# Kernel tuning notes

Measured on AMD Instinct MI355X. Metric: run time of the kernel, lower is better.

The kernel has to match this reference:

```python
import jax, jax.numpy as jnp
import numpy as np

N = 64       # number of nodes (features)
K = 512      # sequence length
WIN = 5
KS = 5       # conv kernel size
EMBED = 64   # embed_dim


def setup_inputs() -> dict:
    key = jax.random.key(0)
    ks = jax.random.split(key, 8)
    x = jax.random.normal(ks[0], (N, K), dtype=jnp.float32)
    # fully connected graph without self loops (remove_self_loops is then a no-op)
    src, dst = np.nonzero(~np.eye(N, dtype=bool))
    edge_index = jnp.asarray(np.stack([src, dst]), dtype=jnp.int32)  # [2, E]
    conv_w = jax.random.normal(ks[1], (1, 1, KS), dtype=jnp.float32) * 0.3
    conv_b = jnp.zeros((1,), jnp.float32)
    s = 1.0 / np.sqrt(WIN)
    lin_l_w = jax.random.uniform(ks[2], (EMBED, WIN), jnp.float32, -s, s)
    lin_l_b = jax.random.uniform(ks[3], (EMBED,), jnp.float32, -s, s)
    lin_r_w = jax.random.uniform(ks[4], (EMBED, WIN), jnp.float32, -s, s)
    lin_r_b = jax.random.uniform(ks[5], (EMBED,), jnp.float32, -s, s)
    glorot = np.sqrt(6.0 / (1 + EMBED))
    att = jax.random.uniform(ks[6], (1, EMBED), jnp.float32, -glorot, glorot)
    return dict(x=x, edge_index=edge_index, conv_w=conv_w, conv_b=conv_b,
                lin_l_w=lin_l_w, lin_l_b=lin_l_b, lin_r_w=lin_r_w,
                lin_r_b=lin_r_b, att=att)


def reference(x, edge_index, conv_w, conv_b, lin_l_w, lin_l_b, lin_r_w, lin_r_b, att):
    n_temp = K - WIN + 1
    # Conv1d(1,1,KS, padding='same') + sigmoid
    h = jax.lax.conv_general_dilated(x[:, None, :], conv_w, window_strides=(1,),
                                     padding='SAME',
                                     dimension_numbers=('NCH', 'OIH', 'NCH'))
    h = jax.nn.sigmoid(h[:, 0, :] + conv_b)                      # [N, K]
    widx = jnp.arange(n_temp)[:, None] + jnp.arange(WIN)[None, :]
    xw = h[:, widx].reshape(-1, WIN)
    # temporal edge index: node idx -> idx*n_temp + t
    t = jnp.arange(n_temp)[None, :]
    l = (edge_index[0][:, None] * n_temp + t).reshape(-1)        # [E*n_temp]
    r = (edge_index[1][:, None] * n_temp + t).reshape(-1)
    x_l = xw @ lin_l_w.T + lin_l_b                               # [N*n_temp, EMBED]
    x_r = xw @ lin_r_w.T + lin_r_b
    e = jax.nn.leaky_relu(x_l[l] + x_r[r], negative_slope=0.2)   # [E*n_temp, EMBED]
    alpha = (e * att).sum(-1)                                    # [E*n_temp]
    # segment softmax grouped by source temporal node l
    S = N * n_temp
    m = jax.ops.segment_max(alpha, l, num_segments=S)
    a = jnp.exp(alpha - m[l])
    denom = jax.ops.segment_sum(a, l, num_segments=S)
    alpha = a / (denom[l] + 1e-16)
    return alpha.reshape(-1, n_temp)                             # [E, n_temp]
```

## Files before the change

kernel.cpp:

```cpp
#include <hip/hip_runtime.h>

#define NNODE 64
#define KLEN  512
#define WIN   5
#define NT    508
#define EMB   64
#define NDST  63

typedef float v2f __attribute__((ext_vector_type(2)));

#define XL_OFF 0

__device__ __forceinline__ int xr_idx(int n, int d) {
    return n * EMB + ((((d >> 2) ^ (n & 7)) << 2) | (d & 3));
}

__device__ __forceinline__ float sigmoid_f(float a) {
    return __builtin_amdgcn_rcpf(1.f + __expf(-a));
}

__global__ __launch_bounds__(256) void precompute_xl(
    const float* __restrict__ x,
    const float* __restrict__ conv_w,
    const float* __restrict__ conv_b,
    const float* __restrict__ lin_l_w,
    const float* __restrict__ lin_l_b,
    float* __restrict__ ws)
{
    const int bx = blockIdx.x;
    const int t  = (bx & 7) * 64 + (bx >> 3);
    if (t >= NT) return;
    const int tid  = threadIdx.x;
    const int lane = tid & 63;
    const int wave = tid >> 6;

    __shared__ float h_s[NNODE][WIN];

    {
        const int n  = tid >> 2;
        const int w0 = tid & 3;
        #pragma unroll
        for (int rep = 0; rep < 2; ++rep) {
            const int w = rep == 0 ? w0 : 4;
            if (rep == 0 || w0 == 0) {
                const int base = t + w - 2;
                float acc = conv_b[0];
                #pragma unroll
                for (int j = 0; j < WIN; ++j) {
                    const int k = base + j;
                    const float xv = (k >= 0 && k < KLEN) ? x[n * KLEN + k] : 0.f;
                    acc = fmaf(conv_w[j], xv, acc);
                }
                h_s[n][w] = sigmoid_f(acc);
            }
        }
    }
    __syncthreads();

    float lw[WIN];
    #pragma unroll
    for (int w = 0; w < WIN; ++w) lw[w] = lin_l_w[lane * WIN + w];
    const float lb = lin_l_b[lane];
    float* xl_ws = ws + XL_OFF + (size_t)t * NNODE * EMB;
    #pragma unroll
    for (int k = 0; k < 16; ++k) {
        const int n = wave + 4 * k;
        float xl = lb;
        #pragma unroll
        for (int w = 0; w < WIN; ++w)
            xl = fmaf(lw[w], h_s[n][w], xl);
        xl_ws[n * EMB + lane] = xl;
    }
}

__global__ __launch_bounds__(256) void attn_main(
    const float* __restrict__ x,
    const float* __restrict__ conv_w,
    const float* __restrict__ conv_b,
    const float* __restrict__ lin_r_w,
    const float* __restrict__ lin_r_b,
    const float* __restrict__ att,
    const float* __restrict__ ws,
    float* __restrict__ out)
{
    const int bx = blockIdx.x;
    const int t  = (bx & 7) * 64 + (bx >> 3);
    if (t >= NT) return;
    const int sg   = blockIdx.y;
    const int tid  = threadIdx.x;
    const int lane = tid & 63;
    const int wave = tid >> 6;

    __shared__ float h_s[NNODE][WIN];
    __shared__ float xr_s[NNODE * EMB];

    {
        const int n  = tid >> 2;
        const int w0 = tid & 3;
        #pragma unroll
        for (int rep = 0; rep < 2; ++rep) {
            const int w = rep == 0 ? w0 : 4;
            if (rep == 0 || w0 == 0) {
                const int base = t + w - 2;
                float acc = conv_b[0];
                #pragma unroll
                for (int j = 0; j < WIN; ++j) {
                    const int k = base + j;
                    const float xv = (k >= 0 && k < KLEN) ? x[n * KLEN + k] : 0.f;
                    acc = fmaf(conv_w[j], xv, acc);
                }
                h_s[n][w] = sigmoid_f(acc);
            }
        }
    }
    __syncthreads();

    {
        float rw[WIN];
        #pragma unroll
        for (int w = 0; w < WIN; ++w) rw[w] = lin_r_w[lane * WIN + w];
        const float rb = lin_r_b[lane];
        #pragma unroll
        for (int k = 0; k < 16; ++k) {
            const int n = wave + 4 * k;
            float xr = rb;
            #pragma unroll
            for (int w = 0; w < WIN; ++w)
                xr = fmaf(rw[w], h_s[n][w], xr);
            xr_s[xr_idx(n, lane)] = xr;
        }
    }

    const int wu = __builtin_amdgcn_readfirstlane(wave);
    const int s0 = sg * 16 + wu * 4;
    const float* xl_g = ws + XL_OFF + (size_t)t * NNODE * EMB + (size_t)s0 * EMB;

    __syncthreads();

    v2f acc2[4], accB2;
    #pragma unroll
    for (int p = 0; p < 4; ++p) acc2[p] = (v2f)(0.f);
    accB2 = (v2f)(0.f);

    float4 xlc[4], xln[4];
    #pragma unroll
    for (int p = 0; p < 4; ++p)
        xlc[p] = *(const float4*)(xl_g + p * EMB);

    #pragma unroll
    for (int d0 = 0; d0 < EMB; d0 += 4) {
        if (d0 + 4 < EMB) {
            #pragma unroll
            for (int p = 0; p < 4; ++p)
                xln[p] = *(const float4*)(xl_g + p * EMB + d0 + 4);
        }
        const float4 xr4 = *(const float4*)&xr_s[xr_idx(lane, d0)];
        const v2f xr01 = {xr4.x, xr4.y};
        const v2f xr23 = {xr4.z, xr4.w};
        const v2f a01  = *(const v2f*)(att + d0);
        const v2f a23  = *(const v2f*)(att + d0 + 2);
        accB2 = __builtin_elementwise_fma(a01, xr01, accB2);
        accB2 = __builtin_elementwise_fma(a23, xr23, accB2);
        #pragma unroll
        for (int p = 0; p < 4; ++p) {
            const v2f xl01 = {xlc[p].x, xlc[p].y};
            const v2f xl23 = {xlc[p].z, xlc[p].w};
            v2f z01 = xl01 + xr01;
            v2f z23 = xl23 + xr23;
            v2f m01 = __builtin_elementwise_max(z01, -z01);
            v2f m23 = __builtin_elementwise_max(z23, -z23);
            acc2[p] = __builtin_elementwise_fma(a01, m01, acc2[p]);
            acc2[p] = __builtin_elementwise_fma(a23, m23, acc2[p]);
        }
        #pragma unroll
        for (int p = 0; p < 4; ++p) xlc[p] = xln[p];
    }
    const float accB = accB2.x + accB2.y;

    float ex[4];
    #pragma unroll
    for (int p = 0; p < 4; ++p) {
        const int s = s0 + p;
        const float alpha = fmaf(0.4f, acc2[p].x + acc2[p].y, 0.6f * accB);
        ex[p] = (lane == s) ? 0.f : __expf(alpha);
    }
    float sum[4];
    #pragma unroll
    for (int p = 0; p < 4; ++p) sum[p] = ex[p];
    #pragma unroll
    for (int off = 32; off; off >>= 1) {
        #pragma unroll
        for (int p = 0; p < 4; ++p) sum[p] += __shfl_xor(sum[p], off);
    }
    #pragma unroll
    for (int p = 0; p < 4; ++p) {
        const int s = s0 + p;
        const float res = ex[p] * __builtin_amdgcn_rcpf(sum[p] + 1e-16f);
        if (lane != s) {
            const int j = lane - (lane > s ? 1 : 0);
            out[(size_t)(s * NDST + j) * NT + t] = res;
        }
    }
}

extern "C" void kernel_launch(void* const* d_in, const int* in_sizes, int n_in,
                              void* d_out, int out_size, void* d_ws, size_t ws_size,
                              hipStream_t stream)
{
    const float* x       = (const float*)d_in[0];
    const float* conv_w  = (const float*)d_in[2];
    const float* conv_b  = (const float*)d_in[3];
    const float* lin_l_w = (const float*)d_in[4];
    const float* lin_l_b = (const float*)d_in[5];
    const float* lin_r_w = (const float*)d_in[6];
    const float* lin_r_b = (const float*)d_in[7];
    const float* att     = (const float*)d_in[8];
    float* out = (float*)d_out;
    float* ws  = (float*)d_ws;

    precompute_xl<<<dim3(512), 256, 0, stream>>>(x, conv_w, conv_b,
        lin_l_w, lin_l_b, ws);
    attn_main<<<dim3(512, 4), 256, 0, stream>>>(x, conv_w, conv_b,
        lin_r_w, lin_r_b, att, ws, out);
}
```

Measured before the change: 29.72 us.

## Precompute conv+sigmoid once into workspace and split x_l build across more blocks

Adds a dedicated conv_h kernel that computes the sigmoid-activated convolution once per (node, position) into workspace, instead of recomputing the windowed conv in every block of both kernels. The x_l builder now reads h from global memory and is split into 4x more blocks, each handling 16 nodes. attn_main also reads h from global instead of recomputing it. This removes redundant conv/exp work and a syncthreads, at the cost of an extra kernel launch and global round-trip for h.

```diff
diff --git a/kernel.cpp b/kernel.cpp
--- a/kernel.cpp
+++ b/kernel.cpp
@@ -9,7 +9,8 @@
 
 typedef float v2f __attribute__((ext_vector_type(2)));
 
-#define XL_OFF 0
+#define H_OFF  0
+#define XL_OFF ((size_t)NNODE * KLEN)
 
 __device__ __forceinline__ int xr_idx(int n, int d) {
     return n * EMB + ((((d >> 2) ^ (n & 7)) << 2) | (d & 3));
@@ -19,64 +20,57 @@
     return __builtin_amdgcn_rcpf(1.f + __expf(-a));
 }
 
-__global__ __launch_bounds__(256) void precompute_xl(
+__global__ __launch_bounds__(256) void conv_h(
     const float* __restrict__ x,
     const float* __restrict__ conv_w,
     const float* __restrict__ conv_b,
+    float* __restrict__ ws)
+{
+    const int n = blockIdx.x >> 1;
+    const int k = ((blockIdx.x & 1) << 8) + threadIdx.x;
+    float acc = conv_b[0];
+    #pragma unroll
+    for (int j = 0; j < WIN; ++j) {
+        const int kk = k + j - 2;
+        const float xv = (kk >= 0 && kk < KLEN) ? x[n * KLEN + kk] : 0.f;
+        acc = fmaf(conv_w[j], xv, acc);
+    }
+    ws[H_OFF + n * KLEN + k] = sigmoid_f(acc);
+}
+
+__global__ __launch_bounds__(256) void build_xl(
     const float* __restrict__ lin_l_w,
     const float* __restrict__ lin_l_b,
     float* __restrict__ ws)
 {
-    const int bx = blockIdx.x;
-    const int t  = (bx & 7) * 64 + (bx >> 3);
+    const int bx  = blockIdx.x;
+    const int t   = (bx & 7) * 64 + ((bx >> 3) >> 2);
     if (t >= NT) return;
+    const int nc  = (bx >> 3) & 3;
     const int tid  = threadIdx.x;
     const int lane = tid & 63;
     const int wave = tid >> 6;
-
-    __shared__ float h_s[NNODE][WIN];
-
-    {
-        const int n  = tid >> 2;
-        const int w0 = tid & 3;
-        #pragma unroll
-        for (int rep = 0; rep < 2; ++rep) {
-            const int w = rep == 0 ? w0 : 4;
-            if (rep == 0 || w0 == 0) {
-                const int base = t + w - 2;
-                float acc = conv_b[0];
-                #pragma unroll
-                for (int j = 0; j < WIN; ++j) {
-                    const int k = base + j;
-                    const float xv = (k >= 0 && k < KLEN) ? x[n * KLEN + k] : 0.f;
-                    acc = fmaf(conv_w[j], xv, acc);
-                }
-                h_s[n][w] = sigmoid_f(acc);
-            }
-        }
-    }
-    __syncthreads();
 
     float lw[WIN];
     #pragma unroll
     for (int w = 0; w < WIN; ++w) lw[w] = lin_l_w[lane * WIN + w];
     const float lb = lin_l_b[lane];
+
+    const float* h_g = ws + H_OFF;
     float* xl_ws = ws + XL_OFF + (size_t)t * NNODE * EMB;
     #pragma unroll
-    for (int k = 0; k < 16; ++k) {
-        const int n = wave + 4 * k;
+    for (int i = 0; i < 4; ++i) {
+        const int n = nc * 16 + wave * 4 + i;
+        const float* hn = h_g + n * KLEN + t;
         float xl = lb;
         #pragma unroll
         for (int w = 0; w < WIN; ++w)
-            xl = fmaf(lw[w], h_s[n][w], xl);
+            xl = fmaf(lw[w], hn[w], xl);
         xl_ws[n * EMB + lane] = xl;
     }
 }
 
 __global__ __launch_bounds__(256) void attn_main(
-    const float* __restrict__ x,
-    const float* __restrict__ conv_w,
-    const float* __restrict__ conv_b,
     const float* __restrict__ lin_r_w,
     const float* __restrict__ lin_r_b,
     const float* __restrict__ att,
@@ -91,42 +85,22 @@
     const int lane = tid & 63;
     const int wave = tid >> 6;
 
-    __shared__ float h_s[NNODE][WIN];
     __shared__ float xr_s[NNODE * EMB];
-
-    {
-        const int n  = tid >> 2;
-        const int w0 = tid & 3;
-        #pragma unroll
-        for (int rep = 0; rep < 2; ++rep) {
-            const int w = rep == 0 ? w0 : 4;
-            if (rep == 0 || w0 == 0) {
-                const int base = t + w - 2;
-                float acc = conv_b[0];
-                #pragma unroll
-                for (int j = 0; j < WIN; ++j) {
-                    const int k = base + j;
-                    const float xv = (k >= 0 && k < KLEN) ? x[n * KLEN + k] : 0.f;
-                    acc = fmaf(conv_w[j], xv, acc);
-                }
-                h_s[n][w] = sigmoid_f(acc);
-            }
-        }
-    }
-    __syncthreads();
 
     {
         float rw[WIN];
         #pragma unroll
         for (int w = 0; w < WIN; ++w) rw[w] = lin_r_w[lane * WIN + w];
         const float rb = lin_r_b[lane];
+        const float* h_g = ws + H_OFF;
         #pragma unroll
         for (int k = 0; k < 16; ++k) {
             const int n = wave + 4 * k;
+            const float* hn = h_g + n * KLEN + t;
             float xr = rb;
             #pragma unroll
             for (int w = 0; w < WIN; ++w)
-                xr = fmaf(rw[w], h_s[n][w], xr);
+                xr = fmaf(rw[w], hn[w], xr);
             xr_s[xr_idx(n, lane)] = xr;
         }
     }
@@ -218,8 +192,7 @@
     float* out = (float*)d_out;
     float* ws  = (float*)d_ws;
 
-    precompute_xl<<<dim3(512), 256, 0, stream>>>(x, conv_w, conv_b,
-        lin_l_w, lin_l_b, ws);
-    attn_main<<<dim3(512, 4), 256, 0, stream>>>(x, conv_w, conv_b,
-        lin_r_w, lin_r_b, att, ws, out);
+    conv_h<<<dim3(128), 256, 0, stream>>>(x, conv_w, conv_b, ws);
+    build_xl<<<dim3(2048), 256, 0, stream>>>(lin_l_w, lin_l_b, ws);
+    attn_main<<<dim3(512, 4), 256, 0, stream>>>(lin_r_w, lin_r_b, att, ws, out);
 }
```

After: 31.57 us. 1.06x slower.
